# Kernel optimization log

Hardware: AMD Instinct MI355X
Metric: run time of the kernel (lower is better)

The kernel has to match this reference:

```python
import jax, jax.numpy as jnp
import numpy as np

B, T, D = 2, 2048, 1024
H, RANK = 16, 32
DH = D // H  # 64


def setup_inputs() -> dict:
    key = jax.random.key(0)
    ks = jax.random.split(key, 6)
    sd = 1.0 / np.sqrt(D)
    sdh = 1.0 / np.sqrt(DH)
    return {
        "x": jax.random.normal(ks[0], (B, T, D), dtype=jnp.float32),
        "W_qkv": jax.random.normal(ks[1], (D, 3 * D), dtype=jnp.float32) * sd,
        "W_q_lsr": jax.random.normal(ks[2], (H, DH, RANK), dtype=jnp.float32) * sdh,
        "W_k_lsr": jax.random.normal(ks[3], (H, DH, RANK), dtype=jnp.float32) * sdh,
        "lsr_core": jnp.ones((H, RANK), dtype=jnp.float32),
        "W_o": jax.random.normal(ks[4], (D, D), dtype=jnp.float32) * sd,
    }


def reference(x, W_qkv, W_q_lsr, W_k_lsr, lsr_core, W_o):
    b, t, d = x.shape
    # Fused QKV projection
    qkv = x @ W_qkv  # (B, T, 3D)
    q, k, v = jnp.split(qkv, 3, axis=-1)
    # (B, H, T, DH)
    q = q.reshape(b, t, H, DH).transpose(0, 2, 1, 3)
    k = k.reshape(b, t, H, DH).transpose(0, 2, 1, 3)
    v = v.reshape(b, t, H, DH).transpose(0, 2, 1, 3)
    # Low-rank bilinear score: q^T Wq diag(core) Wk^T k
    ql = jnp.einsum("bhtd,hdr->bhtr", q, W_q_lsr)  # (B, H, T, R)
    kl = jnp.einsum("bhsd,hdr->bhsr", k, W_k_lsr)  # (B, H, T, R)
    scale = 1.0 / jnp.sqrt(jnp.asarray(RANK, dtype=x.dtype))
    scores = jnp.einsum("bhtr,bhsr->bhts", ql * lsr_core[None, :, None, :], kl) * scale
    # Causal mask
    causal = jnp.tril(jnp.ones((t, t), dtype=bool))
    scores = jnp.where(causal[None, None], scores, jnp.asarray(-jnp.inf, dtype=scores.dtype))
    attn = jax.nn.softmax(scores, axis=-1)
    y = jnp.einsum("bhts,bhsd->bhtd", attn, v)  # (B, H, T, DH)
    y = y.transpose(0, 2, 1, 3).reshape(b, t, d)
    return y @ W_o
```

## Files before the change

kernel.cpp:

```cpp
#include <hip/hip_runtime.h>
#include <hip/hip_bf16.h>

#define B_  2
#define T_  2048
#define D_  1024
#define H_  16
#define DH_ 64
#define R_  32
#define BT_ (B_*T_)
#define BH_ (B_*H_)

typedef unsigned short u16;
typedef unsigned int   u32;
typedef __attribute__((ext_vector_type(8))) short bhalf8;
typedef __attribute__((ext_vector_type(4))) float floatx4;

#define WSB_FLAG  0
#define WSB_XB    256
#define WSB_WCATT (WSB_XB    + 8388608)
#define WSB_QL    (WSB_WCATT + 4194304)
#define WSB_KL    (WSB_QL    + 4194304)
#define WSB_VT    (WSB_KL    + 4194304)
#define WSB_YB    (WSB_VT    + 8388608)
#define WSB_WOT   (WSB_YB    + 8388608)

#define NEG_ -1.0e30f

__device__ __forceinline__ float bfs(u16 s) {
    union { u32 i; float f; } w; w.i = ((u32)s) << 16; return w.f;
}
__device__ __forceinline__ u16 tob(float f) {
    __hip_bfloat16 h = __float2bfloat16(f);
    return *(u16*)&h;
}
__device__ __forceinline__ u32 pack2(float a, float b) {
    return (u32)tob(a) | ((u32)tob(b) << 16);
}
__device__ __forceinline__ void gload16(const u16* g, u16* l) {
    __builtin_amdgcn_global_load_lds(
        (const __attribute__((address_space(1))) void*)g,
        (__attribute__((address_space(3))) void*)l, 16, 0, 0);
}
__device__ __forceinline__ int detect_isbf(const u32* __restrict__ xw, int lane) {
    int hits = 0;
    #pragma unroll
    for (int i = 0; i < 8; ++i) {
        const u32 w = xw[lane + i * 64];
        const u32 h = w & 0xFFFFu;
        const u32 e = (h >> 7) & 0xFFu;
        if (h == 0u || (e >= 100u && e <= 150u)) ++hits;
    }
    #pragma unroll
    for (int off = 32; off; off >>= 1) hits += __shfl_down(hits, off, 64);
    return __shfl(hits, 0, 64) >= 300;
}

__global__ __launch_bounds__(256) void prep_kernel(
    const void* __restrict__ x, u16* __restrict__ xb,
    const void* __restrict__ Wqkv, const void* __restrict__ Wo,
    const void* __restrict__ Wq_lsr, const void* __restrict__ Wk_lsr,
    const void* __restrict__ core,
    u16* __restrict__ WcatT, u16* __restrict__ WoT)
{
    __shared__ __align__(16) u16 Bq[128 * 72];
    __shared__ __align__(16) u16 Bk[128 * 72];
    __shared__ __align__(16) u16 Aq[32 * 72];
    __shared__ __align__(16) u16 Ak[32 * 72];
    const int tid  = threadIdx.x;
    const int lane = tid & 63;
    const int isbf = detect_isbf((const u32*)x, lane);
    const int blk  = blockIdx.x;
    const int w    = tid >> 6;
    const int n16  = lane & 15;
    const int q4   = lane >> 4;

    if (blk < 2048) {
        const int e = blk * 256 + tid;
        if (isbf) {
            ((uint4*)xb)[e] = ((const uint4*)x)[e];
        } else {
            float4 a0 = ((const float4*)x)[2*e];
            float4 a1 = ((const float4*)x)[2*e + 1];
            uint4 o;
            o.x = pack2(a0.x, a0.y); o.y = pack2(a0.z, a0.w);
            o.z = pack2(a1.x, a1.y); o.w = pack2(a1.z, a1.w);
            ((uint4*)xb)[e] = o;
        }
        return;
    }

    if (blk < 2560) {
        int t = blk - 2048;
        const void* src; u16* dst; int srcStride, srcColOff, dstRowOff;
        if (t < 256) { src = Wqkv; dst = WcatT; srcStride = 3*D_; srcColOff = 2*D_; dstRowOff = 1024; }
        else { t -= 256; src = Wo; dst = WoT; srcStride = D_; srcColOff = 0; dstRowOff = 0; }
        const int j0 = (t & 15) * 64;
        const int i0 = (t >> 4) * 64;
        #pragma unroll
        for (int p = 0; p < 2; ++p) {
            const int e = tid + p * 256;
            const int r = e >> 3, ch = e & 7;
            if (isbf) {
                uint4 v = *(const uint4*)((const u16*)src + (size_t)(i0 + r) * srcStride + srcColOff + j0 + ch*8);
                *(uint4*)&Bq[r * 72 + ch*8] = v;
            } else {
                const float* s = (const float*)src + (size_t)(i0 + r) * srcStride + srcColOff + j0 + ch*8;
                float4 a0 = *(const float4*)s;
                float4 a1 = *(const float4*)(s + 4);
                uint4 o;
                o.x = pack2(a0.x, a0.y); o.y = pack2(a0.z, a0.w);
                o.z = pack2(a1.x, a1.y); o.w = pack2(a1.z, a1.w);
                *(uint4*)&Bq[r * 72 + ch*8] = o;
            }
        }
        __syncthreads();
        #pragma unroll
        for (int p = 0; p < 2; ++p) {
            const int e = tid + p * 256;
            const int c = e >> 3, ch = e & 7;
            u16 tmp[8];
            #pragma unroll
            for (int j = 0; j < 8; ++j) tmp[j] = Bq[(ch*8 + j) * 72 + c];
            *(uint4*)(dst + (size_t)(dstRowOff + j0 + c) * D_ + i0 + ch*8) = *(uint4*)tmp;
        }
        return;
    }

    const int fb = blk - 2560;
    const int h  = fb & 15;
    const int d0 = (fb >> 4) * 128;

    #pragma unroll
    for (int p = 0; p < 8; ++p) {
        const int e  = tid + p * 256;
        const int r  = e & 31, dh = e >> 5;
        float aq, ak;
        if (isbf) {
            aq = bfs(((const u16*)Wq_lsr)[(h*DH_ + dh)*R_ + r]);
            ak = bfs(((const u16*)Wk_lsr)[(h*DH_ + dh)*R_ + r]);
        } else {
            aq = ((const float*)Wq_lsr)[(h*DH_ + dh)*R_ + r];
            ak = ((const float*)Wk_lsr)[(h*DH_ + dh)*R_ + r];
        }
        Aq[r * 72 + dh] = tob(aq);
        Ak[r * 72 + dh] = tob(ak);
    }
    #pragma unroll
    for (int p = 0; p < 8; ++p) {
        const int e  = tid + p * 256;
        const int n  = e >> 4, ch = e & 15;
        if (isbf) {
            uint2 wq = *(const uint2*)((const u16*)Wqkv + (size_t)(d0+n)*(3*D_) + h*DH_ + ch*4);
            uint2 wk = *(const uint2*)((const u16*)Wqkv + (size_t)(d0+n)*(3*D_) + D_ + h*DH_ + ch*4);
            *(uint2*)&Bq[n * 72 + ch*4] = wq;
            *(uint2*)&Bk[n * 72 + ch*4] = wk;
        } else {
            float4 fq = *(const float4*)((const float*)Wqkv + (size_t)(d0+n)*(3*D_) + h*DH_ + ch*4);
            float4 fk = *(const float4*)((const float*)Wqkv + (size_t)(d0+n)*(3*D_) + D_ + h*DH_ + ch*4);
            uint2 oq, ok;
            oq.x = pack2(fq.x, fq.y); oq.y = pack2(fq.z, fq.w);
            ok.x = pack2(fk.x, fk.y); ok.y = pack2(fk.z, fk.w);
            *(uint2*)&Bq[n * 72 + ch*4] = oq;
            *(uint2*)&Bk[n * 72 + ch*4] = ok;
        }
    }
    __syncthreads();

    floatx4 accq[2][2], acck[2][2];
    #pragma unroll
    for (int mi = 0; mi < 2; ++mi)
        #pragma unroll
        for (int ni = 0; ni < 2; ++ni) { accq[mi][ni] = (floatx4)(0.f); acck[mi][ni] = (floatx4)(0.f); }

    #pragma unroll
    for (int kk = 0; kk < 2; ++kk) {
        bhalf8 aqf[2], akf[2], bqf[2], bkf[2];
        #pragma unroll
        for (int mi = 0; mi < 2; ++mi) {
            aqf[mi] = *(const bhalf8*)&Aq[(mi*16 + n16) * 72 + kk*32 + q4*8];
            akf[mi] = *(const bhalf8*)&Ak[(mi*16 + n16) * 72 + kk*32 + q4*8];
        }
        #pragma unroll
        for (int ni = 0; ni < 2; ++ni) {
            bqf[ni] = *(const bhalf8*)&Bq[(w*32 + ni*16 + n16) * 72 + kk*32 + q4*8];
            bkf[ni] = *(const bhalf8*)&Bk[(w*32 + ni*16 + n16) * 72 + kk*32 + q4*8];
        }
        #pragma unroll
        for (int mi = 0; mi < 2; ++mi)
            #pragma unroll
            for (int ni = 0; ni < 2; ++ni) {
                accq[mi][ni] = __builtin_amdgcn_mfma_f32_16x16x32_bf16(aqf[mi], bqf[ni], accq[mi][ni], 0, 0, 0);
                acck[mi][ni] = __builtin_amdgcn_mfma_f32_16x16x32_bf16(akf[mi], bkf[ni], acck[mi][ni], 0, 0, 0);
            }
    }

    const float scale = (float)(0.17677669529663687 * 1.4426950408889634);
    #pragma unroll
    for (int mi = 0; mi < 2; ++mi) {
        #pragma unroll
        for (int rr = 0; rr < 4; ++rr) {
            const int r = mi*16 + q4*4 + rr;
            const float cc = (isbf ? bfs(((const u16*)core)[h*R_ + r])
                                   : ((const float*)core)[h*R_ + r]) * scale;
            #pragma unroll
            for (int ni = 0; ni < 2; ++ni) {
                const int d = d0 + w*32 + ni*16 + n16;
                WcatT[(size_t)(h*R_ + r) * D_ + d]       = tob(accq[mi][ni][rr] * cc);
                WcatT[(size_t)(512 + h*R_ + r) * D_ + d] = tob(acck[mi][ni][rr]);
            }
        }
    }
}

__global__ __launch_bounds__(256, 4) void gemm1_mfma(
    const u16* __restrict__ xb, const u16* __restrict__ WcatT,
    u16* __restrict__ ql, u16* __restrict__ kl, u16* __restrict__ vf)
{
    __shared__ __align__(16) u16 As[128 * 64];
    __shared__ __align__(16) u16 Bs[64 * 64];
    const int tid  = threadIdx.x;
    const int lane = tid & 63;
    const int w    = tid >> 6;
    const int n16  = lane & 15;
    const int q4   = lane >> 4;
    const int wx   = w & 1;
    const int wy   = w >> 1;
    const int bm   = blockIdx.y * 128;
    const int bn   = blockIdx.x * 64;
    const int lrow = lane >> 3;
    const int lcol = (lane & 7) * 8;

    floatx4 acc[4][2];
    #pragma unroll
    for (int i = 0; i < 4; ++i)
        #pragma unroll
        for (int j = 0; j < 2; ++j) acc[i][j] = (floatx4)(0.f);

    for (int kt = 0; kt < D_; kt += 64) {
        #pragma unroll
        for (int i = 0; i < 4; ++i) {
            const int r0 = w*32 + i*8;
            gload16(xb + (size_t)(bm + r0 + lrow) * D_ + kt + lcol, &As[r0 * 64]);
        }
        #pragma unroll
        for (int i = 0; i < 2; ++i) {
            const int r0 = w*16 + i*8;
            gload16(WcatT + (size_t)(bn + r0 + lrow) * D_ + kt + lcol, &Bs[r0 * 64]);
        }
        __syncthreads();
        #pragma unroll
        for (int kk = 0; kk < 2; ++kk) {
            bhalf8 a[4], b[2];
            #pragma unroll
            for (int mi = 0; mi < 4; ++mi)
                a[mi] = *(const bhalf8*)&As[(wy*64 + mi*16 + n16) * 64 + kk*32 + q4*8];
            #pragma unroll
            for (int ni = 0; ni < 2; ++ni)
                b[ni] = *(const bhalf8*)&Bs[(wx*32 + ni*16 + n16) * 64 + kk*32 + q4*8];
            #pragma unroll
            for (int mi = 0; mi < 4; ++mi)
                #pragma unroll
                for (int ni = 0; ni < 2; ++ni)
                    acc[mi][ni] = __builtin_amdgcn_mfma_f32_16x16x32_bf16(
                        a[mi], b[ni], acc[mi][ni], 0, 0, 0);
        }
        __syncthreads();
    }

    if (bn < 1024) {
        #pragma unroll
        for (int mi = 0; mi < 4; ++mi) {
            #pragma unroll
            for (int rr = 0; rr < 4; ++rr) {
                const int row = bm + wy*64 + mi*16 + q4*4 + rr;
                const int b   = row >> 11;
                const int t   = row & (T_ - 1);
                #pragma unroll
                for (int ni = 0; ni < 2; ++ni) {
                    const int col = bn + wx*32 + ni*16 + n16;
                    const u16 val = tob(acc[mi][ni][rr]);
                    if (col < 512) {
                        const int h = col >> 5, r = col & 31;
                        ql[((size_t)(b*H_ + h)*T_ + t)*R_ + r] = val;
                    } else {
                        const int c = col - 512; const int h = c >> 5, r = c & 31;
                        kl[((size_t)(b*H_ + h)*T_ + t)*R_ + r] = val;
                    }
                }
            }
        }
    } else {
        #pragma unroll
        for (int mi = 0; mi < 4; ++mi) {
            const int row0 = bm + wy*64 + mi*16 + q4*4;
            const int b  = row0 >> 11;
            const int t  = row0 & (T_ - 1);
            const int tile = t >> 7;
            const int sl   = t & 127;
            const int kc   = sl >> 5;
            const int j2   = (sl >> 4) & 1;
            const int qv   = (sl >> 2) & 3;
            #pragma unroll
            for (int ni = 0; ni < 2; ++ni) {
                const int c  = bn - 1024 + wx*32 + ni*16 + n16;
                const int h  = c >> 6, dh = c & 63;
                const int bh = b*H_ + h;
                const int c2 = dh >> 4;
                const int lv = qv*16 + (dh & 15);
                u16* dst = vf + ((((size_t)bh*16 + tile)*4 + kc)*4 + c2)*512
                              + lv*8 + j2*4;
                uint2 o;
                o.x = pack2(acc[mi][ni][0], acc[mi][ni][1]);
                o.y = pack2(acc[mi][ni][2], acc[mi][ni][3]);
                *(uint2*)dst = o;
            }
        }
    }
}

__device__ __forceinline__ void softmax_update(
    floatx4 (&Sc)[8], float &mrow, float &lrow, floatx4 (&O)[4])
{
    float cmax[8];
    #pragma unroll
    for (int c = 0; c < 8; ++c)
        cmax[c] = fmaxf(fmaxf(Sc[c][0], Sc[c][1]), fmaxf(Sc[c][2], Sc[c][3]));
    float rmax = fmaxf(fmaxf(fmaxf(cmax[0], cmax[1]), fmaxf(cmax[2], cmax[3])),
                       fmaxf(fmaxf(cmax[4], cmax[5]), fmaxf(cmax[6], cmax[7])));
    rmax = fmaxf(rmax, __shfl_xor(rmax, 16, 64));
    rmax = fmaxf(rmax, __shfl_xor(rmax, 32, 64));

    const float mn = fmaxf(mrow, rmax);
    const int norescale = __all(rmax <= mrow);

    float csum[8];
    #pragma unroll
    for (int c = 0; c < 8; ++c) {
        #pragma unroll
        for (int r = 0; r < 4; ++r)
            Sc[c][r] = __builtin_amdgcn_exp2f(Sc[c][r] - mn);
        csum[c] = (Sc[c][0] + Sc[c][1]) + (Sc[c][2] + Sc[c][3]);
    }
    float rsum = ((csum[0] + csum[1]) + (csum[2] + csum[3]))
               + ((csum[4] + csum[5]) + (csum[6] + csum[7]));
    rsum += __shfl_xor(rsum, 16, 64);
    rsum += __shfl_xor(rsum, 32, 64);

    if (norescale) {
        lrow += rsum;
    } else {
        const float alpha = __builtin_amdgcn_exp2f(mrow - mn);
        mrow = mn;
        lrow = lrow * alpha + rsum;
        #pragma unroll
        for (int c2 = 0; c2 < 4; ++c2)
            #pragma unroll
            for (int r = 0; r < 4; ++r) O[c2][r] *= alpha;
    }
}

__global__ __launch_bounds__(512, 4) void attn_kernel(
    const u16* __restrict__ ql, const u16* __restrict__ kl,
    const u16* __restrict__ vf, u16* __restrict__ y)
{
    __shared__ __align__(16) u16 kls[128 * 40];
    __shared__ __align__(16) u16 vsT[2][8192];

    const int tid  = threadIdx.x;
    const int lane = tid & 63;
    const int w    = tid >> 6;
    const int n16  = lane & 15;
    const int q4   = lane >> 4;
    const int bh   = blockIdx.x;
    const int by   = blockIdx.y;
    const int qt2  = (by < 8) ? (15 - by) : (by - 8);
    const int t0   = qt2 * 128;
    const int nt   = qt2 + 1;

    const u16* qlb = ql + (size_t)bh * T_ * R_;
    const bhalf8 aq = *(const bhalf8*)(qlb + (size_t)(t0 + w*16 + n16) * R_ + q4*8);

    const u16* klb = kl + (size_t)bh * T_ * R_;
    const u16* vfb = vf + (size_t)bh * 131072;
    const int rk = tid >> 2, ck = (tid & 3) * 8;

    uint4 kc0 = *(const uint4*)(klb + (size_t)rk * R_ + ck);
    uint4 kn0 = kc0;
    gload16(vfb + (size_t)(w*2    ) * 512 + lane*8, &vsT[0][(w*2    ) * 512]);
    gload16(vfb + (size_t)(w*2 + 1) * 512 + lane*8, &vsT[0][(w*2 + 1) * 512]);

    float mrow = NEG_, lrow = 0.f;
    floatx4 O[4];
    #pragma unroll
    for (int c = 0; c < 4; ++c) O[c] = (floatx4)(0.f);

    for (int it = 0; it < nt; ++it) {
        const int cur = it & 1;
        __syncthreads();
        *(uint4*)&kls[rk * 40 + ck] = kc0;
        __syncthreads();
        if (it + 1 < nt) {
            const u16* vnb = vfb + (size_t)(it + 1) * 8192;
            gload16(vnb + (size_t)(w*2    ) * 512 + lane*8, &vsT[cur ^ 1][(w*2    ) * 512]);
            gload16(vnb + (size_t)(w*2 + 1) * 512 + lane*8, &vsT[cur ^ 1][(w*2 + 1) * 512]);
            kn0 = *(const uint4*)(klb + (size_t)((it+1)*128 + rk) * R_ + ck);
        }

        floatx4 Sc[8];
        #pragma unroll
        for (int c = 0; c < 8; ++c) {
            bhalf8 ak = *(const bhalf8*)&kls[(16*c + n16) * 40 + q4*8];
            Sc[c] = __builtin_amdgcn_mfma_f32_16x16x32_bf16(ak, aq, (floatx4)(0.f), 0, 0, 0);
        }

        if (it == nt - 1) {
            const int tq = w*16 + n16;
            #pragma unroll
            for (int c = 0; c < 8; ++c) {
                const int sb = 16*c + 4*q4;
                #pragma unroll
                for (int r = 0; r < 4; ++r)
                    if (sb + r > tq) Sc[c][r] = NEG_;
            }
        }

        softmax_update(Sc, mrow, lrow, O);

        const u16* vt = &vsT[cur][lane * 8];
        #pragma unroll
        for (int kc = 0; kc < 4; ++kc) {
            union { u32 wd[4]; bhalf8 v; } pu;
            pu.wd[0] = pack2(Sc[2*kc    ][0], Sc[2*kc    ][1]);
            pu.wd[1] = pack2(Sc[2*kc    ][2], Sc[2*kc    ][3]);
            pu.wd[2] = pack2(Sc[2*kc + 1][0], Sc[2*kc + 1][1]);
            pu.wd[3] = pack2(Sc[2*kc + 1][2], Sc[2*kc + 1][3]);
            const bhalf8 pa = pu.v;
            #pragma unroll
            for (int c2 = 0; c2 < 4; ++c2) {
                bhalf8 bv = *(const bhalf8*)(vt + (size_t)(kc*4 + c2) * 512);
                O[c2] = __builtin_amdgcn_mfma_f32_16x16x32_bf16(bv, pa, O[c2], 0, 0, 0);
            }
        }

        kc0 = kn0;
    }

    const int b = bh >> 4, h = bh & 15;
    const float rl = 1.0f / lrow;
    const int t = t0 + w*16 + n16;
    u16* yr = y + ((size_t)b * T_ + t) * D_ + h * DH_;
    #pragma unroll
    for (int c2 = 0; c2 < 4; ++c2) {
        uint2 o;
        o.x = pack2(O[c2][0] * rl, O[c2][1] * rl);
        o.y = pack2(O[c2][2] * rl, O[c2][3] * rl);
        *(uint2*)(yr + 16*c2 + 4*q4) = o;
    }
}

__global__ __launch_bounds__(256, 4) void out_gemm_mfma(
    const u16* __restrict__ yb, const u16* __restrict__ WoT,
    float* __restrict__ out)
{
    __shared__ __align__(16) u16 As[64 * 64];
    __shared__ __align__(16) u16 Bs[64 * 64];
    const int tid  = threadIdx.x;
    const int lane = tid & 63;
    const int w    = tid >> 6;
    const int n16  = lane & 15;
    const int q4   = lane >> 4;
    const int wx   = w & 1;
    const int wy   = w >> 1;
    const int bm   = blockIdx.y * 64;
    const int bn   = blockIdx.x * 64;
    const int lrow = lane >> 3;
    const int lcol = (lane & 7) * 8;

    floatx4 acc[2][2];
    #pragma unroll
    for (int i = 0; i < 2; ++i)
        #pragma unroll
        for (int j = 0; j < 2; ++j) acc[i][j] = (floatx4)(0.f);

    for (int kt = 0; kt < D_; kt += 64) {
        #pragma unroll
        for (int i = 0; i < 2; ++i) {
            const int r0 = w*16 + i*8;
            gload16(yb  + (size_t)(bm + r0 + lrow) * D_ + kt + lcol, &As[r0 * 64]);
            gload16(WoT + (size_t)(bn + r0 + lrow) * D_ + kt + lcol, &Bs[r0 * 64]);
        }
        __syncthreads();
        #pragma unroll
        for (int kk = 0; kk < 2; ++kk) {
            bhalf8 a[2], b[2];
            #pragma unroll
            for (int mi = 0; mi < 2; ++mi)
                a[mi] = *(const bhalf8*)&As[(wy*32 + mi*16 + n16) * 64 + kk*32 + q4*8];
            #pragma unroll
            for (int ni = 0; ni < 2; ++ni)
                b[ni] = *(const bhalf8*)&Bs[(wx*32 + ni*16 + n16) * 64 + kk*32 + q4*8];
            #pragma unroll
            for (int mi = 0; mi < 2; ++mi)
                #pragma unroll
                for (int ni = 0; ni < 2; ++ni)
                    acc[mi][ni] = __builtin_amdgcn_mfma_f32_16x16x32_bf16(
                        a[mi], b[ni], acc[mi][ni], 0, 0, 0);
        }
        __syncthreads();
    }

    #pragma unroll
    for (int mi = 0; mi < 2; ++mi) {
        #pragma unroll
        for (int rr = 0; rr < 4; ++rr) {
            const int row = bm + wy*32 + mi*16 + q4*4 + rr;
            #pragma unroll
            for (int ni = 0; ni < 2; ++ni) {
                const int col = bn + wx*32 + ni*16 + n16;
                out[(size_t)row * D_ + col] = acc[mi][ni][rr];
            }
        }
    }
}

extern "C" void kernel_launch(void* const* d_in, const int* in_sizes, int n_in,
                              void* d_out, int out_size, void* d_ws, size_t ws_size,
                              hipStream_t stream)
{
    (void)out_size; (void)ws_size;
    const void* in_x = nullptr; const void* in_wqkv = nullptr;
    const void* in_wq = nullptr; const void* in_wk = nullptr;
    const void* in_core = nullptr; const void* in_wo = nullptr;
    for (int i = 0; i < n_in; ++i) {
        const int s = in_sizes[i];
        if      (s == BT_*D_)     { if (!in_x)    in_x    = d_in[i]; }
        else if (s == D_*3*D_)    { if (!in_wqkv) in_wqkv = d_in[i]; }
        else if (s == H_*DH_*R_)  { if (!in_wq)   in_wq   = d_in[i]; else if (!in_wk) in_wk = d_in[i]; }
        else if (s == H_*R_)      { if (!in_core) in_core = d_in[i]; }
        else if (s == D_*D_)      { if (!in_wo)   in_wo   = d_in[i]; }
    }
    if (!in_x)    in_x    = d_in[0];
    if (!in_wqkv) in_wqkv = d_in[1];
    if (!in_wq)   in_wq   = d_in[2];
    if (!in_wk)   in_wk   = d_in[3];
    if (!in_core) in_core = d_in[4];
    if (!in_wo)   in_wo   = d_in[5];

    float* out = (float*)d_out;

    char* ws    = (char*)d_ws;
    u16*  xb    = (u16*)(ws + WSB_XB);
    u16*  WcatT = (u16*)(ws + WSB_WCATT);
    u16*  ql    = (u16*)(ws + WSB_QL);
    u16*  kl    = (u16*)(ws + WSB_KL);
    u16*  vf    = (u16*)(ws + WSB_VT);
    u16*  yb    = (u16*)(ws + WSB_YB);
    u16*  WoT   = (u16*)(ws + WSB_WOT);

    prep_kernel<<<2688, 256, 0, stream>>>(in_x, xb, in_wqkv, in_wo,
                                          in_wq, in_wk, in_core, WcatT, WoT);
    gemm1_mfma<<<dim3(32, 32), 256, 0, stream>>>(xb, WcatT, ql, kl, vf);
    attn_kernel<<<dim3(32, 16), 512, 0, stream>>>(ql, kl, vf, yb);
    out_gemm_mfma<<<dim3(16, 64), 256, 0, stream>>>(yb, WoT, out);
}
```

Before: 176.5 us.

## Store K in pre-swizzled tiles loaded direct-to-LDS and remap GEMM blocks per XCD

The QKV GEMM now writes the K low-rank projection in a tiled, XOR-swizzled layout so the attention kernel can fetch each K tile with direct global-to-LDS loads into a double buffer. This removes the register round-trip and the second barrier per iteration. Both GEMMs also switch to a 1D grid whose block index is remapped so that consecutive tiles land on the same XCD, aiming for better L2 reuse. The swizzle has to match exactly between writer and reader, and the scattered K stores in the GEMM epilogue may cost a little more.

```diff
diff --git a/kernel.cpp b/kernel.cpp
--- a/kernel.cpp
+++ b/kernel.cpp
@@ -19,8 +19,8 @@
 #define WSB_XB    256
 #define WSB_WCATT (WSB_XB    + 8388608)
 #define WSB_QL    (WSB_WCATT + 4194304)
-#define WSB_KL    (WSB_QL    + 4194304)
-#define WSB_VT    (WSB_KL    + 4194304)
+#define WSB_KF    (WSB_QL    + 4194304)
+#define WSB_VT    (WSB_KF    + 4194304)
 #define WSB_YB    (WSB_VT    + 8388608)
 #define WSB_WOT   (WSB_YB    + 8388608)
 
@@ -214,7 +214,7 @@
 
 __global__ __launch_bounds__(256, 4) void gemm1_mfma(
     const u16* __restrict__ xb, const u16* __restrict__ WcatT,
-    u16* __restrict__ ql, u16* __restrict__ kl, u16* __restrict__ vf)
+    u16* __restrict__ ql, u16* __restrict__ kf, u16* __restrict__ vf)
 {
     __shared__ __align__(16) u16 As[128 * 64];
     __shared__ __align__(16) u16 Bs[64 * 64];
@@ -225,8 +225,10 @@
     const int q4   = lane >> 4;
     const int wx   = w & 1;
     const int wy   = w >> 1;
-    const int bm   = blockIdx.y * 128;
-    const int bn   = blockIdx.x * 64;
+    const int bid  = blockIdx.x;
+    const int lid  = (bid & 7) * 128 + (bid >> 3);
+    const int bm   = (lid >> 5) * 128;
+    const int bn   = (lid & 31) * 64;
     const int lrow = lane >> 3;
     const int lcol = (lane & 7) * 8;
 
@@ -284,7 +286,9 @@
                         ql[((size_t)(b*H_ + h)*T_ + t)*R_ + r] = val;
                     } else {
                         const int c = col - 512; const int h = c >> 5, r = c & 31;
-                        kl[((size_t)(b*H_ + h)*T_ + t)*R_ + r] = val;
+                        const int bh = b*H_ + h;
+                        kf[((size_t)bh*16 + (t >> 7)) * 4096
+                           + (size_t)(t & 127) * 32 + (r ^ (rr << 3))] = val;
                     }
                 }
             }
@@ -360,10 +364,10 @@
 }
 
 __global__ __launch_bounds__(512, 4) void attn_kernel(
-    const u16* __restrict__ ql, const u16* __restrict__ kl,
+    const u16* __restrict__ ql, const u16* __restrict__ kf,
     const u16* __restrict__ vf, u16* __restrict__ y)
 {
-    __shared__ __align__(16) u16 kls[128 * 40];
+    __shared__ __align__(16) u16 kls[2][4096];
     __shared__ __align__(16) u16 vsT[2][8192];
 
     const int tid  = threadIdx.x;
@@ -380,14 +384,14 @@
     const u16* qlb = ql + (size_t)bh * T_ * R_;
     const bhalf8 aq = *(const bhalf8*)(qlb + (size_t)(t0 + w*16 + n16) * R_ + q4*8);
 
-    const u16* klb = kl + (size_t)bh * T_ * R_;
+    const u16* kfb = kf + (size_t)bh * 65536;
     const u16* vfb = vf + (size_t)bh * 131072;
-    const int rk = tid >> 2, ck = (tid & 3) * 8;
-
-    uint4 kc0 = *(const uint4*)(klb + (size_t)rk * R_ + ck);
-    uint4 kn0 = kc0;
+
+    gload16(kfb + (size_t)w * 512 + lane*8,        &kls[0][w * 512]);
     gload16(vfb + (size_t)(w*2    ) * 512 + lane*8, &vsT[0][(w*2    ) * 512]);
     gload16(vfb + (size_t)(w*2 + 1) * 512 + lane*8, &vsT[0][(w*2 + 1) * 512]);
+
+    const int kbase = n16*32 + ((q4 ^ (n16 & 3)) * 8);
 
     float mrow = NEG_, lrow = 0.f;
     floatx4 O[4];
@@ -397,19 +401,19 @@
     for (int it = 0; it < nt; ++it) {
         const int cur = it & 1;
         __syncthreads();
-        *(uint4*)&kls[rk * 40 + ck] = kc0;
-        __syncthreads();
         if (it + 1 < nt) {
-            const u16* vnb = vfb + (size_t)(it + 1) * 8192;
-            gload16(vnb + (size_t)(w*2    ) * 512 + lane*8, &vsT[cur ^ 1][(w*2    ) * 512]);
-            gload16(vnb + (size_t)(w*2 + 1) * 512 + lane*8, &vsT[cur ^ 1][(w*2 + 1) * 512]);
-            kn0 = *(const uint4*)(klb + (size_t)((it+1)*128 + rk) * R_ + ck);
+            const u16* kn = kfb + (size_t)(it + 1) * 4096;
+            const u16* vn = vfb + (size_t)(it + 1) * 8192;
+            gload16(kn + (size_t)w * 512 + lane*8,        &kls[cur ^ 1][w * 512]);
+            gload16(vn + (size_t)(w*2    ) * 512 + lane*8, &vsT[cur ^ 1][(w*2    ) * 512]);
+            gload16(vn + (size_t)(w*2 + 1) * 512 + lane*8, &vsT[cur ^ 1][(w*2 + 1) * 512]);
         }
 
         floatx4 Sc[8];
+        const u16* kb = &kls[cur][kbase];
         #pragma unroll
         for (int c = 0; c < 8; ++c) {
-            bhalf8 ak = *(const bhalf8*)&kls[(16*c + n16) * 40 + q4*8];
+            bhalf8 ak = *(const bhalf8*)(kb + c * 512);
             Sc[c] = __builtin_amdgcn_mfma_f32_16x16x32_bf16(ak, aq, (floatx4)(0.f), 0, 0, 0);
         }
 
@@ -441,8 +445,6 @@
                 O[c2] = __builtin_amdgcn_mfma_f32_16x16x32_bf16(bv, pa, O[c2], 0, 0, 0);
             }
         }
-
-        kc0 = kn0;
     }
 
     const int b = bh >> 4, h = bh & 15;
@@ -471,8 +473,10 @@
     const int q4   = lane >> 4;
     const int wx   = w & 1;
     const int wy   = w >> 1;
-    const int bm   = blockIdx.y * 64;
-    const int bn   = blockIdx.x * 64;
+    const int bid  = blockIdx.x;
+    const int lid  = (bid & 7) * 128 + (bid >> 3);
+    const int bm   = (lid >> 4) * 64;
+    const int bn   = (lid & 15) * 64;
     const int lrow = lane >> 3;
     const int lcol = (lane & 7) * 8;
 
@@ -552,14 +556,14 @@
     u16*  xb    = (u16*)(ws + WSB_XB);
     u16*  WcatT = (u16*)(ws + WSB_WCATT);
     u16*  ql    = (u16*)(ws + WSB_QL);
-    u16*  kl    = (u16*)(ws + WSB_KL);
+    u16*  kf    = (u16*)(ws + WSB_KF);
     u16*  vf    = (u16*)(ws + WSB_VT);
     u16*  yb    = (u16*)(ws + WSB_YB);
     u16*  WoT   = (u16*)(ws + WSB_WOT);
 
     prep_kernel<<<2688, 256, 0, stream>>>(in_x, xb, in_wqkv, in_wo,
                                           in_wq, in_wk, in_core, WcatT, WoT);
-    gemm1_mfma<<<dim3(32, 32), 256, 0, stream>>>(xb, WcatT, ql, kl, vf);
-    attn_kernel<<<dim3(32, 16), 512, 0, stream>>>(ql, kl, vf, yb);
-    out_gemm_mfma<<<dim3(16, 64), 256, 0, stream>>>(yb, WoT, out);
-}
+    gemm1_mfma<<<1024, 256, 0, stream>>>(xb, WcatT, ql, kf, vf);
+    attn_kernel<<<dim3(32, 16), 512, 0, stream>>>(ql, kf, vf, yb);
+    out_gemm_mfma<<<1024, 256, 0, stream>>>(yb, WoT, out);
+}
```

Measured after the change: 180.3 us. +2.2%, slower.
